# Kernel optimization log

Measured on AMD Instinct MI355X. Metric: run time of the kernel, lower is better.

Reference implementation:

```python
import jax, jax.numpy as jnp
import numpy as np

FEAT_SIZE, HIDDEN_SIZE, ATT_SIZE = 2048, 1024, 512
BATCH, FEAT_NUM = 64, 512


def setup_inputs() -> dict:
    key = jax.random.key(0)
    ks = jax.random.split(key, 8)
    s = lambda fan_in: 1.0 / np.sqrt(fan_in)
    return {
        "feats": jax.random.normal(ks[0], (BATCH, FEAT_NUM, FEAT_SIZE), jnp.float32),
        "key": jax.random.normal(ks[1], (BATCH, HIDDEN_SIZE), jnp.float32),
        "wh_w": jax.random.uniform(ks[2], (ATT_SIZE, HIDDEN_SIZE), jnp.float32, -s(HIDDEN_SIZE), s(HIDDEN_SIZE)),
        "wh_b": jax.random.uniform(ks[3], (ATT_SIZE,), jnp.float32, -s(HIDDEN_SIZE), s(HIDDEN_SIZE)),
        "wv_w": jax.random.uniform(ks[4], (ATT_SIZE, FEAT_SIZE), jnp.float32, -s(FEAT_SIZE), s(FEAT_SIZE)),
        "wv_b": jax.random.uniform(ks[5], (ATT_SIZE,), jnp.float32, -s(FEAT_SIZE), s(FEAT_SIZE)),
        "wa_w": jax.random.uniform(ks[6], (1, ATT_SIZE), jnp.float32, -s(ATT_SIZE), s(ATT_SIZE)),
    }


def reference(feats, key, wh_w, wh_b, wv_w, wv_b, wa_w):
    # v = wv(feats): (B, N, A)
    v = jnp.einsum('bnf,af->bna', feats, wv_w) + wv_b
    # h = wh(key): (B, A), broadcast-added over feat_num
    h = key @ wh_w.T + wh_b
    inputs = h[:, None, :] + v                       # (B, N, A)
    scores = jnp.einsum('bna,a->bn', jnp.tanh(inputs), wa_w[0])  # (B, N)
    alpha = jax.nn.softmax(scores, axis=1)           # (B, N)
    att_feats = jnp.einsum('bn,bnf->bf', alpha, feats)  # (B, F)
    return (att_feats, alpha)
```

## Files before the change

### kernel.cpp

```cpp
#include <hip/hip_runtime.h>
#include <hip/hip_bf16.h>

#define FEATSZ 2048
#define HIDSZ  1024
#define ATTSZ  512
#define BATCH  64
#define FEATN  512

typedef float  f32x4  __attribute__((ext_vector_type(4)));
typedef __bf16 bf16x8 __attribute__((ext_vector_type(8)));

__device__ __forceinline__ unsigned short f2bf(float f) {
    union { float f; unsigned int u; } x; x.f = f;
    unsigned int u = x.u;
    return (unsigned short)((u + 0x7fffu + ((u >> 16) & 1u)) >> 16);
}

__global__ void k_h(const float* __restrict__ key, const float* __restrict__ wh_w,
                    const float* __restrict__ wh_b, float* __restrict__ h) {
    const int b = blockIdx.y;
    const int ac = blockIdx.x;
    const int t = threadIdx.x;
    const int lane = t & 63, wv = t >> 6;
    float k16[16];
    const float* kb = key + b * HIDSZ;
#pragma unroll
    for (int j = 0; j < 16; ++j) k16[j] = kb[lane + 64 * j];
#pragma unroll 1
    for (int i = 0; i < 16; ++i) {
        int a = ac * 64 + wv * 16 + i;
        const float* wr = wh_w + (size_t)a * HIDSZ;
        float s = 0.f;
#pragma unroll
        for (int j = 0; j < 16; ++j) s += k16[j] * wr[lane + 64 * j];
#pragma unroll
        for (int d = 32; d; d >>= 1) s += __shfl_xor(s, d);
        if (lane == 0) h[b * ATTSZ + a] = s + wh_b[a];
    }
}

__global__ void k_wvcvt(const float* __restrict__ wv_w, unsigned short* __restrict__ wvb) {
    int idx = blockIdx.x * 256 + threadIdx.x;
    int a = idx >> 11, k = idx & 2047;
    int CF = a >> 4, c = a & 15, ks = k >> 5, kin = k & 31;
    int lane = c + ((kin >> 3) << 4);
    int dst = ((ks * 32 + CF) * 64 + lane) * 8 + (kin & 7);
    wvb[dst] = f2bf(wv_w[idx]);
}

__global__ __launch_bounds__(512) void k_scores(
        const float* __restrict__ feats, const unsigned short* __restrict__ wvb,
        const float* __restrict__ h, const float* __restrict__ wv_b,
        const float* __restrict__ wa, float* __restrict__ part_sc) {
    __shared__ __align__(16) char Abuf[2][32768];
    __shared__ float scp[4][256];
    const int t = threadIdx.x, lane = t & 63, w = t >> 6;
    const int wm = w >> 2, wn = w & 3;
    const int mb = blockIdx.x >> 1, nt = blockIdx.x & 1;
    const int m0 = mb * 256, b = blockIdx.x >> 2;

    const float* gbase = feats + (size_t)(m0 + (t >> 3)) * FEATSZ + (t & 7) * 8;
    const int woff = ((t >> 3) * 128) + ((((t & 7) ^ ((t >> 3) & 7))) * 16);

    const unsigned short* wbase = wvb + (size_t)(nt * 16 + wn * 4) * 512 + lane * 8;

    const int arow = wm * 128 + (lane & 15);
    const int aq = lane >> 4, ax = lane & 7;

    f32x4 acc[8][4];
#pragma unroll
    for (int m = 0; m < 8; ++m)
#pragma unroll
        for (int cf = 0; cf < 4; ++cf) acc[m][cf] = (f32x4)0.0f;

    bf16x8 BA[4], BB[4];
    f32x4 G0a, G0b, G1a, G1b, G2a, G2b, G3a, G3b;

    auto issueG = [&](int kt, int p, f32x4& ga, f32x4& gb) {
        const float* s = gbase + (size_t)p * (64 * FEATSZ) + kt * 64;
        ga = *(const f32x4*)s;
        gb = *(const f32x4*)(s + 4);
    };
    auto loadB = [&](bf16x8(&B)[4], int kkg) {
#pragma unroll
        for (int cf = 0; cf < 4; ++cf)
            B[cf] = *(const bf16x8*)(wbase + (size_t)(kkg * 32 + cf) * 512);
    };
    auto cvtWrite = [&](char* bw, int p, f32x4 ga, f32x4 gb) {
        bf16x8 v;
        v[0] = (__bf16)ga[0]; v[1] = (__bf16)ga[1]; v[2] = (__bf16)ga[2]; v[3] = (__bf16)ga[3];
        v[4] = (__bf16)gb[0]; v[5] = (__bf16)gb[1]; v[6] = (__bf16)gb[2]; v[7] = (__bf16)gb[3];
        *(bf16x8*)__builtin_assume_aligned(bw + p * 8192 + woff, 16) = v;
    };
    auto mfmaPhase = [&](const char* br, int mg, int kk, bf16x8(&B)[4]) {
        bf16x8 a0 = *(const bf16x8*)__builtin_assume_aligned(br + (arow + (mg + 0) * 16) * 128 + (((kk * 4 + aq) ^ ax) * 16), 16);
        bf16x8 a1 = *(const bf16x8*)__builtin_assume_aligned(br + (arow + (mg + 1) * 16) * 128 + (((kk * 4 + aq) ^ ax) * 16), 16);
        bf16x8 a2 = *(const bf16x8*)__builtin_assume_aligned(br + (arow + (mg + 2) * 16) * 128 + (((kk * 4 + aq) ^ ax) * 16), 16);
        bf16x8 a3 = *(const bf16x8*)__builtin_assume_aligned(br + (arow + (mg + 3) * 16) * 128 + (((kk * 4 + aq) ^ ax) * 16), 16);
        __builtin_amdgcn_s_setprio(1);
#pragma unroll
        for (int cf = 0; cf < 4; ++cf) acc[mg + 0][cf] = __builtin_amdgcn_mfma_f32_16x16x32_bf16(a0, B[cf], acc[mg + 0][cf], 0, 0, 0);
#pragma unroll
        for (int cf = 0; cf < 4; ++cf) acc[mg + 1][cf] = __builtin_amdgcn_mfma_f32_16x16x32_bf16(a1, B[cf], acc[mg + 1][cf], 0, 0, 0);
#pragma unroll
        for (int cf = 0; cf < 4; ++cf) acc[mg + 2][cf] = __builtin_amdgcn_mfma_f32_16x16x32_bf16(a2, B[cf], acc[mg + 2][cf], 0, 0, 0);
#pragma unroll
        for (int cf = 0; cf < 4; ++cf) acc[mg + 3][cf] = __builtin_amdgcn_mfma_f32_16x16x32_bf16(a3, B[cf], acc[mg + 3][cf], 0, 0, 0);
        __builtin_amdgcn_s_setprio(0);
        __builtin_amdgcn_sched_barrier(0);
    };

    issueG(0, 0, G0a, G0b); issueG(0, 1, G1a, G1b);
    issueG(0, 2, G2a, G2b); issueG(0, 3, G3a, G3b);
    loadB(BA, 0);
    cvtWrite(&Abuf[0][0], 0, G0a, G0b);
    cvtWrite(&Abuf[0][0], 1, G1a, G1b);
    cvtWrite(&Abuf[0][0], 2, G2a, G2b);
    cvtWrite(&Abuf[0][0], 3, G3a, G3b);
    issueG(1, 0, G0a, G0b); issueG(1, 1, G1a, G1b);
    issueG(1, 2, G2a, G2b); issueG(1, 3, G3a, G3b);
    __syncthreads();

#pragma unroll 1
    for (int kt = 0; kt < 32; ++kt) {
        const char* br = &Abuf[kt & 1][0];
        char* bw = &Abuf[(kt & 1) ^ 1][0];
        loadB(BB, kt * 2 + 1);
        if (kt < 31) cvtWrite(bw, 0, G0a, G0b);
        if (kt < 30) issueG(kt + 2, 0, G0a, G0b);
        mfmaPhase(br, 0, 0, BA);
        if (kt < 31) cvtWrite(bw, 1, G1a, G1b);
        if (kt < 30) issueG(kt + 2, 1, G1a, G1b);
        mfmaPhase(br, 4, 0, BA);
        if (kt < 31) loadB(BA, (kt + 1) * 2);
        if (kt < 31) cvtWrite(bw, 2, G2a, G2b);
        if (kt < 30) issueG(kt + 2, 2, G2a, G2b);
        mfmaPhase(br, 0, 1, BB);
        if (kt < 31) cvtWrite(bw, 3, G3a, G3b);
        if (kt < 30) issueG(kt + 2, 3, G3a, G3b);
        mfmaPhase(br, 4, 1, BB);
        asm volatile("s_waitcnt lgkmcnt(0)" ::: "memory");
        __builtin_amdgcn_s_barrier();
        __builtin_amdgcn_sched_barrier(0);
    }

    const int c16 = lane & 15, q4 = lane >> 4;
    float hreg[4], wreg[4];
#pragma unroll
    for (int cf = 0; cf < 4; ++cf) {
        int a = nt * 256 + wn * 64 + cf * 16 + c16;
        hreg[cf] = h[b * ATTSZ + a] + wv_b[a];
        wreg[cf] = wa[a];
    }
    float pv[8][4];
#pragma unroll
    for (int m = 0; m < 8; ++m)
#pragma unroll
        for (int jr = 0; jr < 4; ++jr) pv[m][jr] = 0.f;
#pragma unroll
    for (int m = 0; m < 8; ++m)
#pragma unroll
        for (int cf = 0; cf < 4; ++cf)
#pragma unroll
            for (int jr = 0; jr < 4; ++jr)
                pv[m][jr] += tanhf(acc[m][cf][jr] + hreg[cf]) * wreg[cf];
#pragma unroll
    for (int m = 0; m < 8; ++m)
#pragma unroll
        for (int jr = 0; jr < 4; ++jr) {
            float v = pv[m][jr];
            v += __shfl_xor(v, 1); v += __shfl_xor(v, 2);
            v += __shfl_xor(v, 4); v += __shfl_xor(v, 8);
            pv[m][jr] = v;
        }
    if (c16 == 0) {
#pragma unroll
        for (int m = 0; m < 8; ++m)
#pragma unroll
            for (int jr = 0; jr < 4; ++jr)
                scp[wn][wm * 128 + m * 16 + q4 * 4 + jr] = pv[m][jr];
    }
    __syncthreads();
    if (t < 256)
        part_sc[nt * (BATCH * FEATN) + m0 + t]
            = scp[0][t] + scp[1][t] + scp[2][t] + scp[3][t];
}

__global__ void k_softmax(const float* __restrict__ part_sc, float* __restrict__ alpha) {
    __shared__ float red[16];
    const int b = blockIdx.x, t = threadIdx.x;
    const int lane = t & 63, w = t >> 6;
    const int r = b * FEATN + t;
    float s = part_sc[r] + part_sc[BATCH * FEATN + r];
    float m = s;
#pragma unroll
    for (int d = 32; d; d >>= 1) m = fmaxf(m, __shfl_xor(m, d));
    if (lane == 0) red[w] = m;
    __syncthreads();
    if (t == 0) {
        float mm = red[0];
        for (int i = 1; i < 8; ++i) mm = fmaxf(mm, red[i]);
        red[8] = mm;
    }
    __syncthreads();
    float e = __expf(s - red[8]);
    float sum = e;
#pragma unroll
    for (int d = 32; d; d >>= 1) sum += __shfl_xor(sum, d);
    if (lane == 0) red[w] = sum;
    __syncthreads();
    if (t == 0) {
        float ss = 0.f;
        for (int i = 0; i < 8; ++i) ss += red[i];
        red[9] = 1.0f / ss;
    }
    __syncthreads();
    alpha[b * FEATN + t] = e * red[9];
}

__global__ void k_att_part(const float* __restrict__ feats, const float* __restrict__ alpha,
                           float* __restrict__ part) {
    const int b = blockIdx.x, fc = blockIdx.y, ns = blockIdx.z, t = threadIdx.x;
    const int f0 = fc * 1024 + t * 4;
    const float* fp = feats + (size_t)(b * FEATN + ns * 128) * FEATSZ + f0;
    const float* al = alpha + b * FEATN + ns * 128;
    float4 acc = {0.f, 0.f, 0.f, 0.f};
#pragma unroll 4
    for (int i = 0; i < 128; ++i) {
        float a = al[i];
        float4 v = *(const float4*)(fp + (size_t)i * FEATSZ);
        acc.x += a * v.x; acc.y += a * v.y; acc.z += a * v.z; acc.w += a * v.w;
    }
    *(float4*)(part + ((size_t)ns * BATCH + b) * FEATSZ + f0) = acc;
}

__global__ void k_att_red(const float* __restrict__ part, float* __restrict__ out) {
    const int idx = (blockIdx.x * 256 + threadIdx.x) * 4;
    float4 s = *(const float4*)(part + idx);
#pragma unroll
    for (int z = 1; z < 4; ++z) {
        float4 v = *(const float4*)(part + (size_t)z * (BATCH * FEATSZ) + idx);
        s.x += v.x; s.y += v.y; s.z += v.z; s.w += v.w;
    }
    *(float4*)(out + idx) = s;
}

extern "C" void kernel_launch(void* const* d_in, const int* in_sizes, int n_in,
                              void* d_out, int out_size, void* d_ws, size_t ws_size,
                              hipStream_t stream) {
    const float* feats = (const float*)d_in[0];
    const float* key   = (const float*)d_in[1];
    const float* wh_w  = (const float*)d_in[2];
    const float* wh_b  = (const float*)d_in[3];
    const float* wv_w  = (const float*)d_in[4];
    const float* wv_b  = (const float*)d_in[5];
    const float* wa_w  = (const float*)d_in[6];

    float* out_att   = (float*)d_out;
    float* out_alpha = out_att + BATCH * FEATSZ;

    char* ws = (char*)d_ws;
    float* h            = (float*)(ws);
    float* part_sc      = (float*)(ws + 131072);
    unsigned short* wvb = (unsigned short*)(ws + 393216);
    float* part         = (float*)(ws + 393216);

    hipLaunchKernelGGL(k_h,        dim3(8, 64),    dim3(256), 0, stream, key, wh_w, wh_b, h);
    hipLaunchKernelGGL(k_wvcvt,    dim3(4096),     dim3(256), 0, stream, wv_w, wvb);
    hipLaunchKernelGGL(k_scores,   dim3(256),      dim3(512), 0, stream, feats, wvb, h, wv_b, wa_w, part_sc);
    hipLaunchKernelGGL(k_softmax,  dim3(64),       dim3(512), 0, stream, part_sc, out_alpha);
    hipLaunchKernelGGL(k_att_part, dim3(64, 2, 4), dim3(256), 0, stream, feats, out_alpha, part);
    hipLaunchKernelGGL(k_att_red,  dim3(128),      dim3(256), 0, stream, part, out_att);
}
```

Baseline: 165.5 us.

## Restructure feats staging to per-thread 32-float runs with barrier-phased MFMA pipeline

Each thread now loads a contiguous 32-float half-row of the feats tile instead of 8 floats across four row groups, using a matching swizzled LDS write pattern. The main loop is reorganised into four phases. In each phase the LDS A fragments are read up front, global loads and conversion writes are interleaved, and a workgroup barrier precedes each MFMA burst, in a ping-pong style schedule. This aims to overlap global and LDS traffic with MFMA work across waves. It adds more barriers per iteration and changes the global access coalescing pattern.

```diff
diff --git a/kernel.cpp b/kernel.cpp
--- a/kernel.cpp
+++ b/kernel.cpp
@@ -59,8 +59,12 @@
     const int mb = blockIdx.x >> 1, nt = blockIdx.x & 1;
     const int m0 = mb * 256, b = blockIdx.x >> 2;
 
-    const float* gbase = feats + (size_t)(m0 + (t >> 3)) * FEATSZ + (t & 7) * 8;
-    const int woff = ((t >> 3) * 128) + ((((t & 7) ^ ((t >> 3) & 7))) * 16);
+    const int sr = t >> 1, sh = t & 1;
+    const float* gbase = feats + (size_t)(m0 + sr) * FEATSZ + sh * 32;
+    int wq[4];
+#pragma unroll
+    for (int q = 0; q < 4; ++q)
+        wq[q] = sr * 128 + (((sh * 4 + q) ^ (sr & 7)) * 16);
 
     const unsigned short* wbase = wvb + (size_t)(nt * 16 + wn * 4) * 512 + lane * 8;
 
@@ -73,75 +77,85 @@
 #pragma unroll
         for (int cf = 0; cf < 4; ++cf) acc[m][cf] = (f32x4)0.0f;
 
-    bf16x8 BA[4], BB[4];
-    f32x4 G0a, G0b, G1a, G1b, G2a, G2b, G3a, G3b;
-
-    auto issueG = [&](int kt, int p, f32x4& ga, f32x4& gb) {
-        const float* s = gbase + (size_t)p * (64 * FEATSZ) + kt * 64;
-        ga = *(const f32x4*)s;
-        gb = *(const f32x4*)(s + 4);
+    bf16x8 BX[4], BY[4];
+    f32x4 FH0, FH1, FH2, FH3, SH0, SH1, SH2, SH3;
+
+    auto ldG = [&](int kt, int i) -> f32x4 {
+        return *(const f32x4*)(gbase + kt * 64 + i * 4);
     };
     auto loadB = [&](bf16x8(&B)[4], int kkg) {
 #pragma unroll
         for (int cf = 0; cf < 4; ++cf)
             B[cf] = *(const bf16x8*)(wbase + (size_t)(kkg * 32 + cf) * 512);
     };
-    auto cvtWrite = [&](char* bw, int p, f32x4 ga, f32x4 gb) {
+    auto cvtW = [&](char* bw, int q, f32x4 a, f32x4 c) {
         bf16x8 v;
-        v[0] = (__bf16)ga[0]; v[1] = (__bf16)ga[1]; v[2] = (__bf16)ga[2]; v[3] = (__bf16)ga[3];
-        v[4] = (__bf16)gb[0]; v[5] = (__bf16)gb[1]; v[6] = (__bf16)gb[2]; v[7] = (__bf16)gb[3];
-        *(bf16x8*)__builtin_assume_aligned(bw + p * 8192 + woff, 16) = v;
-    };
-    auto mfmaPhase = [&](const char* br, int mg, int kk, bf16x8(&B)[4]) {
-        bf16x8 a0 = *(const bf16x8*)__builtin_assume_aligned(br + (arow + (mg + 0) * 16) * 128 + (((kk * 4 + aq) ^ ax) * 16), 16);
-        bf16x8 a1 = *(const bf16x8*)__builtin_assume_aligned(br + (arow + (mg + 1) * 16) * 128 + (((kk * 4 + aq) ^ ax) * 16), 16);
-        bf16x8 a2 = *(const bf16x8*)__builtin_assume_aligned(br + (arow + (mg + 2) * 16) * 128 + (((kk * 4 + aq) ^ ax) * 16), 16);
-        bf16x8 a3 = *(const bf16x8*)__builtin_assume_aligned(br + (arow + (mg + 3) * 16) * 128 + (((kk * 4 + aq) ^ ax) * 16), 16);
+        v[0] = (__bf16)a[0]; v[1] = (__bf16)a[1]; v[2] = (__bf16)a[2]; v[3] = (__bf16)a[3];
+        v[4] = (__bf16)c[0]; v[5] = (__bf16)c[1]; v[6] = (__bf16)c[2]; v[7] = (__bf16)c[3];
+        *(bf16x8*)__builtin_assume_aligned(bw + wq[q], 16) = v;
+    };
+    auto dsr4 = [&](const char* br, int mg, int kk, bf16x8(&A)[4]) {
+#pragma unroll
+        for (int i = 0; i < 4; ++i)
+            A[i] = *(const bf16x8*)__builtin_assume_aligned(
+                br + (arow + (mg + i) * 16) * 128 + (((kk * 4 + aq) ^ ax) * 16), 16);
+    };
+    auto mfma16 = [&](int mg, bf16x8(&A)[4], bf16x8(&B)[4]) {
         __builtin_amdgcn_s_setprio(1);
 #pragma unroll
-        for (int cf = 0; cf < 4; ++cf) acc[mg + 0][cf] = __builtin_amdgcn_mfma_f32_16x16x32_bf16(a0, B[cf], acc[mg + 0][cf], 0, 0, 0);
-#pragma unroll
-        for (int cf = 0; cf < 4; ++cf) acc[mg + 1][cf] = __builtin_amdgcn_mfma_f32_16x16x32_bf16(a1, B[cf], acc[mg + 1][cf], 0, 0, 0);
-#pragma unroll
-        for (int cf = 0; cf < 4; ++cf) acc[mg + 2][cf] = __builtin_amdgcn_mfma_f32_16x16x32_bf16(a2, B[cf], acc[mg + 2][cf], 0, 0, 0);
-#pragma unroll
-        for (int cf = 0; cf < 4; ++cf) acc[mg + 3][cf] = __builtin_amdgcn_mfma_f32_16x16x32_bf16(a3, B[cf], acc[mg + 3][cf], 0, 0, 0);
+        for (int m = 0; m < 4; ++m)
+#pragma unroll
+            for (int cf = 0; cf < 4; ++cf)
+                acc[mg + m][cf] = __builtin_amdgcn_mfma_f32_16x16x32_bf16(A[m], B[cf], acc[mg + m][cf], 0, 0, 0);
         __builtin_amdgcn_s_setprio(0);
+    };
+    auto barIssue = [&]() {
         __builtin_amdgcn_sched_barrier(0);
-    };
-
-    issueG(0, 0, G0a, G0b); issueG(0, 1, G1a, G1b);
-    issueG(0, 2, G2a, G2b); issueG(0, 3, G3a, G3b);
-    loadB(BA, 0);
-    cvtWrite(&Abuf[0][0], 0, G0a, G0b);
-    cvtWrite(&Abuf[0][0], 1, G1a, G1b);
-    cvtWrite(&Abuf[0][0], 2, G2a, G2b);
-    cvtWrite(&Abuf[0][0], 3, G3a, G3b);
-    issueG(1, 0, G0a, G0b); issueG(1, 1, G1a, G1b);
-    issueG(1, 2, G2a, G2b); issueG(1, 3, G3a, G3b);
-    __syncthreads();
+        __builtin_amdgcn_s_barrier();
+        asm volatile("s_waitcnt lgkmcnt(0)" ::: "memory");
+        __builtin_amdgcn_sched_barrier(0);
+    };
+
+    FH0 = ldG(0, 0); FH1 = ldG(0, 1); FH2 = ldG(0, 2); FH3 = ldG(0, 3);
+    SH0 = ldG(0, 4); SH1 = ldG(0, 5); SH2 = ldG(0, 6); SH3 = ldG(0, 7);
+    loadB(BX, 0);
+    cvtW(&Abuf[0][0], 0, FH0, FH1); cvtW(&Abuf[0][0], 1, FH2, FH3);
+    cvtW(&Abuf[0][0], 2, SH0, SH1); cvtW(&Abuf[0][0], 3, SH2, SH3);
+    FH0 = ldG(1, 0); FH1 = ldG(1, 1); FH2 = ldG(1, 2); FH3 = ldG(1, 3);
+    asm volatile("s_waitcnt lgkmcnt(0)" ::: "memory");
+    __builtin_amdgcn_s_barrier();
 
 #pragma unroll 1
     for (int kt = 0; kt < 32; ++kt) {
         const char* br = &Abuf[kt & 1][0];
         char* bw = &Abuf[(kt & 1) ^ 1][0];
-        loadB(BB, kt * 2 + 1);
-        if (kt < 31) cvtWrite(bw, 0, G0a, G0b);
-        if (kt < 30) issueG(kt + 2, 0, G0a, G0b);
-        mfmaPhase(br, 0, 0, BA);
-        if (kt < 31) cvtWrite(bw, 1, G1a, G1b);
-        if (kt < 30) issueG(kt + 2, 1, G1a, G1b);
-        mfmaPhase(br, 4, 0, BA);
-        if (kt < 31) loadB(BA, (kt + 1) * 2);
-        if (kt < 31) cvtWrite(bw, 2, G2a, G2b);
-        if (kt < 30) issueG(kt + 2, 2, G2a, G2b);
-        mfmaPhase(br, 0, 1, BB);
-        if (kt < 31) cvtWrite(bw, 3, G3a, G3b);
-        if (kt < 30) issueG(kt + 2, 3, G3a, G3b);
-        mfmaPhase(br, 4, 1, BB);
-        asm volatile("s_waitcnt lgkmcnt(0)" ::: "memory");
-        __builtin_amdgcn_s_barrier();
-        __builtin_amdgcn_sched_barrier(0);
+        bf16x8 A0[4], A1[4], A2[4], A3[4];
+        dsr4(br, 0, 0, A0);
+        if (kt < 31) { SH0 = ldG(kt + 1, 4); SH1 = ldG(kt + 1, 5); }
+        loadB(BY, kt * 2 + 1);
+        barIssue();
+        mfma16(0, A0, BX);
+        __builtin_amdgcn_s_barrier();
+        dsr4(br, 4, 0, A1);
+        if (kt < 31) {
+            cvtW(bw, 0, FH0, FH1); cvtW(bw, 1, FH2, FH3);
+            SH2 = ldG(kt + 1, 6); SH3 = ldG(kt + 1, 7);
+        }
+        barIssue();
+        mfma16(4, A1, BX);
+        __builtin_amdgcn_s_barrier();
+        dsr4(br, 0, 1, A2);
+        if (kt < 30) { FH0 = ldG(kt + 2, 0); FH1 = ldG(kt + 2, 1); }
+        if (kt < 31) loadB(BX, (kt + 1) * 2);
+        barIssue();
+        mfma16(0, A2, BY);
+        __builtin_amdgcn_s_barrier();
+        dsr4(br, 4, 1, A3);
+        if (kt < 31) { cvtW(bw, 2, SH0, SH1); cvtW(bw, 3, SH2, SH3); }
+        if (kt < 30) { FH2 = ldG(kt + 2, 2); FH3 = ldG(kt + 2, 3); }
+        barIssue();
+        mfma16(4, A3, BY);
+        __builtin_amdgcn_s_barrier();
     }
 
     const int c16 = lane & 15, q4 = lane >> 4;
```

Result: slower. 318.1 us (+92.2%).
